# Kernel tuning notes

Measured on AMD Instinct MI355X. Metric: run time of the kernel, lower is better.

The kernel has to match this reference:

```python
import jax, jax.numpy as jnp
import numpy as np

BATCH = 16
N_ROIS = 1000
NUM_CLASSES = 81
DET_MAX = 100
MIN_CONF = 0.7
NMS_THRESH = 0.3
BBOX_STD = jnp.array([0.1, 0.1, 0.2, 0.2], jnp.float32)


def setup_inputs() -> dict:
    key = jax.random.key(0)
    k1, k2, k3, k4, k5 = jax.random.split(key, 5)
    # valid normalized boxes (y1,x1,y2,x2) with y2>y1, x2>x1
    y1 = jax.random.uniform(k1, (BATCH, N_ROIS, 1)) * 0.7
    x1 = jax.random.uniform(k2, (BATCH, N_ROIS, 1)) * 0.7
    hw = jax.random.uniform(k3, (BATCH, N_ROIS, 2)) * 0.28 + 0.02
    rois = jnp.concatenate([y1, x1, y1 + hw[..., :1], x1 + hw[..., 1:]], axis=-1)
    fpn_class = jax.nn.softmax(jax.random.normal(k4, (BATCH, N_ROIS, NUM_CLASSES)) * 2.0, axis=-1)
    fpn_bbox = jax.random.normal(k5, (BATCH, N_ROIS, NUM_CLASSES, 4)) * 0.1
    window = jnp.tile(jnp.array([[0.0, 0.0, 1.0, 1.0]], jnp.float32), (BATCH, 1))
    return {"rois": rois, "fpn_class": fpn_class, "fpn_bbox": fpn_bbox, "window": window}


def apply_box_deltas(boxes, deltas):
    # boxes [N,4] (y1,x1,y2,x2), deltas [N,4] (dy,dx,log dh,log dw)
    h = boxes[:, 2] - boxes[:, 0]
    w = boxes[:, 3] - boxes[:, 1]
    cy = boxes[:, 0] + 0.5 * h
    cx = boxes[:, 1] + 0.5 * w
    cy = cy + deltas[:, 0] * h
    cx = cx + deltas[:, 1] * w
    h = h * jnp.exp(deltas[:, 2])
    w = w * jnp.exp(deltas[:, 3])
    y1 = cy - 0.5 * h
    x1 = cx - 0.5 * w
    return jnp.stack([y1, x1, y1 + h, x1 + w], axis=1)


def clip_boxes(boxes, window):
    wy1, wx1, wy2, wx2 = window[0], window[1], window[2], window[3]
    y1 = jnp.clip(boxes[:, 0], wy1, wy2)
    x1 = jnp.clip(boxes[:, 1], wx1, wx2)
    y2 = jnp.clip(boxes[:, 2], wy1, wy2)
    x2 = jnp.clip(boxes[:, 3], wx1, wx2)
    return jnp.stack([y1, x1, y2, x2], axis=1)


def box_iou(a, b):
    # a [N,4], b [M,4] -> [N,M]
    y1 = jnp.maximum(a[:, None, 0], b[None, :, 0])
    x1 = jnp.maximum(a[:, None, 1], b[None, :, 1])
    y2 = jnp.minimum(a[:, None, 2], b[None, :, 2])
    x2 = jnp.minimum(a[:, None, 3], b[None, :, 3])
    inter = jnp.maximum(y2 - y1, 0.0) * jnp.maximum(x2 - x1, 0.0)
    area_a = (a[:, 2] - a[:, 0]) * (a[:, 3] - a[:, 1])
    area_b = (b[:, 2] - b[:, 0]) * (b[:, 3] - b[:, 1])
    union = area_a[:, None] + area_b[None, :] - inter
    return inter / jnp.maximum(union, 1e-10)


def per_class_nms_mask(boxes, class_ids, scores):
    """boxes [N,4], class_ids [N] int, scores [N] (already -1 where pre-filtered).
    Returns bool [N]: survives greedy per-class NMS (max DET_MAX kept per class)."""
    fg = jnp.arange(1, NUM_CLASSES)                       # [C-1] skip background
    sc = jnp.where(class_ids[None, :] == fg[:, None], scores[None, :], -1.0)  # [C-1,N]
    order = jnp.argsort(-sc, axis=1)                      # [C-1,N] score-desc per class
    iou = box_iou(boxes, boxes)                           # [N,N]
    col = jnp.arange(N_ROIS)
    active0 = sc >= 0.0
    kept0 = jnp.zeros_like(active0)
    cnt0 = jnp.zeros((NUM_CLASSES - 1,), jnp.int32)

    def body(i, carry):
        active, kept, cnt = carry
        cur = order[:, i]                                  # [C-1] current box idx per class
        is_act = jnp.take_along_axis(active, cur[:, None], axis=1)[:, 0]
        is_kept = is_act & (cnt < DET_MAX)
        cnt = cnt + is_kept.astype(jnp.int32)
        kept = kept | ((col[None, :] == cur[:, None]) & is_kept[:, None])
        suppress = is_kept[:, None] & (iou[cur] > NMS_THRESH)  # [C-1,N]
        active = active & ~suppress
        return (active, kept, cnt)

    _, kept, _ = jax.lax.fori_loop(0, N_ROIS, body, (active0, kept0, cnt0))
    return kept.any(axis=0)


def _refine_one(rois, probs, deltas, window):
    n = jnp.arange(N_ROIS)
    class_ids = jnp.argmax(probs, axis=1)                 # [N]
    class_scores = probs[n, class_ids]                    # [N]
    d = deltas[n, class_ids] * BBOX_STD                   # [N,4]
    refined = clip_boxes(apply_box_deltas(rois, d), window)
    keep = (class_ids > 0) & (class_scores >= MIN_CONF)
    sg = jax.lax.stop_gradient
    nms_keep = per_class_nms_mask(
        sg(refined), class_ids, jnp.where(keep, sg(class_scores), -1.0))
    keep = keep & nms_keep
    sf = jnp.where(keep, class_scores, -1.0)
    top_s, top_i = jax.lax.top_k(sf, DET_MAX)             # keep top DET_MAX overall
    valid = top_s >= 0.0
    det = jnp.concatenate(
        [refined[top_i],
         class_ids[top_i][:, None].astype(jnp.float32),
         class_scores[top_i][:, None]], axis=1)           # [DET_MAX,6]
    return jnp.where(valid[:, None], det, 0.0)            # zero-pad invalid rows


def reference(rois, fpn_class, fpn_bbox, window):
    # [B, DET_MAX, 6] = (y1,x1,y2,x2,class_id,score), normalized coords
    return jax.vmap(_refine_one)(rois, fpn_class, fpn_bbox, window)
```

## Files before the change

### kernel.cpp

```cpp
#include <hip/hip_runtime.h>
#include <math.h>

#define BATCH 16
#define N_ROIS 1000
#define NUM_CLASSES 81
#define DET_MAX 100
#define MIN_CONF 0.7f
#define NMS_THRESH 0.3f

#define ROI_TILE 128
#define SUP_WORDS 4

__global__ __launch_bounds__(256) void refine_v4(
    const float* __restrict__ rois, const float* __restrict__ probs,
    const float* __restrict__ deltas, const float* __restrict__ window,
    float* __restrict__ ws_box, float* __restrict__ ws_score, int* __restrict__ ws_cls)
{
    __shared__ float s_probs[ROI_TILE * NUM_CLASSES];

    const int base_roi = blockIdx.x * ROI_TILE;

    const float4* src = (const float4*)(probs + (size_t)base_roi * NUM_CLASSES);
    float4* dst = (float4*)s_probs;
    for (int i = threadIdx.x; i < ROI_TILE * NUM_CLASSES / 4; i += 256)
        dst[i] = src[i];
    __syncthreads();

    if (threadIdx.x < ROI_TILE) {
        const int idx = base_roi + threadIdx.x;
        const int b = idx / N_ROIS;

        const float* p = s_probs + threadIdx.x * NUM_CLASSES;
        float bs0 = p[0], bs1 = p[1], bs2 = p[2], bs3 = p[3];
        int ib0 = 0, ib1 = 1, ib2 = 2, ib3 = 3;
        #pragma unroll
        for (int c = 4; c <= 76; c += 4) {
            float v0 = p[c], v1 = p[c + 1], v2 = p[c + 2], v3 = p[c + 3];
            if (v0 > bs0) { bs0 = v0; ib0 = c; }
            if (v1 > bs1) { bs1 = v1; ib1 = c + 1; }
            if (v2 > bs2) { bs2 = v2; ib2 = c + 2; }
            if (v3 > bs3) { bs3 = v3; ib3 = c + 3; }
        }
        { float v = p[80]; if (v > bs0) { bs0 = v; ib0 = 80; } }
        if (bs1 > bs0 || (bs1 == bs0 && ib1 < ib0)) { bs0 = bs1; ib0 = ib1; }
        if (bs3 > bs2 || (bs3 == bs2 && ib3 < ib2)) { bs2 = bs3; ib2 = ib3; }
        if (bs2 > bs0 || (bs2 == bs0 && ib2 < ib0)) { bs0 = bs2; ib0 = ib2; }
        const float bs = bs0;
        const int best = ib0;

        const bool keep = (best > 0) && (bs >= MIN_CONF);
        ws_score[idx] = keep ? bs : -1.0f;

        if (keep) {
            const float4 dd = ((const float4*)deltas)[(size_t)idx * NUM_CLASSES + best];
            float dy = dd.x * 0.1f, dx = dd.y * 0.1f, dh = dd.z * 0.2f, dw = dd.w * 0.2f;

            const float4 rr = ((const float4*)rois)[idx];
            float y1 = rr.x, x1 = rr.y, y2 = rr.z, x2 = rr.w;
            float h = y2 - y1, w = x2 - x1;
            float cy = y1 + 0.5f * h, cx = x1 + 0.5f * w;
            cy += dy * h;
            cx += dx * w;
            h *= expf(dh);
            w *= expf(dw);
            float ny1 = cy - 0.5f * h;
            float nx1 = cx - 0.5f * w;
            float ny2 = ny1 + h;
            float nx2 = nx1 + w;

            const float* win = window + b * 4;
            float wy1 = win[0], wx1 = win[1], wy2 = win[2], wx2 = win[3];
            ny1 = fminf(fmaxf(ny1, wy1), wy2);
            nx1 = fminf(fmaxf(nx1, wx1), wx2);
            ny2 = fminf(fmaxf(ny2, wy1), wy2);
            nx2 = fminf(fmaxf(nx2, wx1), wx2);

            ((float4*)ws_box)[idx] = make_float4(ny1, nx1, ny2, nx2);
            ws_cls[idx] = best;
        }
    }
}

__global__ __launch_bounds__(256) void nms_v5(
    const float* __restrict__ ws_box, const float* __restrict__ ws_score,
    const int* __restrict__ ws_cls, float* __restrict__ out)
{
    const int b = blockIdx.x;
    const int tid = threadIdx.x;

    __shared__ float s_cbox[N_ROIS][4];
    __shared__ float s_csc[N_ROIS];
    __shared__ short s_cidx[N_ROIS];
    __shared__ unsigned char s_ccls[N_ROIS];
    __shared__ float s_sbox[N_ROIS][4];
    __shared__ float s_ssc[N_ROIS];
    __shared__ unsigned char s_scls[N_ROIS];
    __shared__ unsigned char s_kept[N_ROIS];
    __shared__ short s_bucket[N_ROIS];
    __shared__ short s_pos[N_ROIS];
    __shared__ unsigned long long s_sup[N_ROIS][SUP_WORDS];
    __shared__ int s_cnt[NUM_CLASSES];
    __shared__ int s_off[NUM_CLASSES];
    __shared__ int s_C;

    if (tid == 0) s_C = 0;
    if (tid < NUM_CLASSES) s_cnt[tid] = 0;

    for (int i = tid; i < DET_MAX * 6; i += 256)
        out[(size_t)b * DET_MAX * 6 + i] = 0.0f;
    __syncthreads();

    for (int i = tid; i < N_ROIS; i += 256) {
        float sc = ws_score[b * N_ROIS + i];
        if (sc >= 0.0f) {
            int k = atomicAdd(&s_C, 1);
            s_csc[k] = sc;
            s_cidx[k] = (short)i;
            int c = ws_cls[b * N_ROIS + i];
            s_ccls[k] = (unsigned char)c;
            atomicAdd(&s_cnt[c], 1);
            float4 bb = ((const float4*)ws_box)[b * N_ROIS + i];
            s_cbox[k][0] = bb.x; s_cbox[k][1] = bb.y;
            s_cbox[k][2] = bb.z; s_cbox[k][3] = bb.w;
        }
    }
    __syncthreads();
    const int C = s_C;

    if (tid == 0) {
        int acc = 0;
        for (int c = 0; c < NUM_CLASSES; ++c) { s_off[c] = acc; acc += s_cnt[c]; }
    }
    __syncthreads();

    for (int k = tid; k < C; k += 256) {
        float sk = s_csc[k];
        int ik = s_cidx[k];
        int ck = s_ccls[k];
        int rank = 0, crank = 0;
        for (int j = 0; j < C; ++j) {
            float sj = s_csc[j];
            int before = (sj > sk) | ((sj == sk) & (s_cidx[j] < ik));
            rank += before;
            crank += before & (s_ccls[j] == ck);
        }
        s_ssc[rank] = sk;
        s_scls[rank] = (unsigned char)ck;
        s_sbox[rank][0] = s_cbox[k][0];
        s_sbox[rank][1] = s_cbox[k][1];
        s_sbox[rank][2] = s_cbox[k][2];
        s_sbox[rank][3] = s_cbox[k][3];
        s_kept[rank] = 0;
        s_pos[rank] = (short)crank;
        s_bucket[s_off[ck] + crank] = (short)rank;
    }
    __syncthreads();

    for (int u = tid; u < C; u += 256) {
        const int i = s_bucket[u];
        const int c = s_scls[i];
        const int m = s_cnt[c];
        if (m > 64 * SUP_WORDS) continue;
        const int a = s_pos[i];
        const int off = u - a;
        const float b0 = s_sbox[i][0], b1 = s_sbox[i][1];
        const float b2 = s_sbox[i][2], b3 = s_sbox[i][3];
        const float area_b = (b2 - b0) * (b3 - b1);
        #pragma unroll
        for (int qw = 0; qw < SUP_WORDS; ++qw) {
            unsigned long long w = 0;
            const int qlo = (qw << 6) > (a + 1) ? (qw << 6) : (a + 1);
            const int qhi = m < ((qw << 6) + 64) ? m : ((qw << 6) + 64);
            for (int q = qlo; q < qhi; ++q) {
                const int j = s_bucket[off + q];
                const float a0 = s_sbox[j][0], a1 = s_sbox[j][1];
                const float a2 = s_sbox[j][2], a3 = s_sbox[j][3];
                float yy1 = fmaxf(a0, b0);
                float xx1 = fmaxf(a1, b1);
                float yy2 = fminf(a2, b2);
                float xx2 = fminf(a3, b3);
                float inter = fmaxf(yy2 - yy1, 0.0f) * fmaxf(xx2 - xx1, 0.0f);
                float area_a = (a2 - a0) * (a3 - a1);
                float uni = area_a + area_b - inter;
                w |= (unsigned long long)(inter / fmaxf(uni, 1e-10f) > NMS_THRESH)
                     << (q & 63);
            }
            s_sup[u][qw] = w;
        }
    }
    __syncthreads();

    if (tid >= 1 && tid < NUM_CLASSES) {
        const int off = s_off[tid];
        const int m = s_cnt[tid];
        if (m <= 64 * SUP_WORDS) {
            unsigned long long r0 = 0, r1 = 0, r2 = 0, r3 = 0;
            int cnt = 0;
            for (int a = 0; a < m; ++a) {
                if (cnt >= DET_MAX) break;
                const unsigned long long rb =
                    (a < 64) ? r0 : (a < 128) ? r1 : (a < 192) ? r2 : r3;
                if ((rb >> (a & 63)) & 1ull) continue;
                const int i = s_bucket[off + a];
                s_kept[i] = 1; ++cnt;
                r0 |= s_sup[off + a][0];
                r1 |= s_sup[off + a][1];
                r2 |= s_sup[off + a][2];
                r3 |= s_sup[off + a][3];
            }
        } else {
            int kept_cnt = 0;
            for (int a = 0; a < m; ++a) {
                if (kept_cnt >= DET_MAX) break;
                int i = s_bucket[off + a];
                float b0 = s_sbox[i][0], b1 = s_sbox[i][1];
                float b2 = s_sbox[i][2], b3 = s_sbox[i][3];
                float area_b = (b2 - b0) * (b3 - b1);
                bool sup = false;
                for (int q = 0; q < a; ++q) {
                    int j = s_bucket[off + q];
                    if (!s_kept[j]) continue;
                    float a0 = s_sbox[j][0], a1 = s_sbox[j][1];
                    float a2 = s_sbox[j][2], a3 = s_sbox[j][3];
                    float yy1 = fmaxf(a0, b0);
                    float xx1 = fmaxf(a1, b1);
                    float yy2 = fminf(a2, b2);
                    float xx2 = fminf(a3, b3);
                    float inter = fmaxf(yy2 - yy1, 0.0f) * fmaxf(xx2 - xx1, 0.0f);
                    float area_a = (a2 - a0) * (a3 - a1);
                    float uni = area_a + area_b - inter;
                    if (inter / fmaxf(uni, 1e-10f) > NMS_THRESH) { sup = true; break; }
                }
                if (!sup) { s_kept[i] = 1; ++kept_cnt; }
            }
        }
    }
    __syncthreads();

    for (int i = tid; i < C; i += 256) {
        if (s_kept[i]) {
            int slot = 0;
            for (int j = 0; j < i; ++j) slot += s_kept[j];
            if (slot < DET_MAX) {
                float* o = out + (size_t)b * DET_MAX * 6 + slot * 6;
                o[0] = s_sbox[i][0];
                o[1] = s_sbox[i][1];
                o[2] = s_sbox[i][2];
                o[3] = s_sbox[i][3];
                o[4] = (float)s_scls[i];
                o[5] = s_ssc[i];
            }
        }
    }
}

extern "C" void kernel_launch(void* const* d_in, const int* in_sizes, int n_in,
                              void* d_out, int out_size, void* d_ws, size_t ws_size,
                              hipStream_t stream) {
    const float* rois      = (const float*)d_in[0];
    const float* fpn_class = (const float*)d_in[1];
    const float* fpn_bbox  = (const float*)d_in[2];
    const float* window    = (const float*)d_in[3];
    float* out = (float*)d_out;

    float* ws_box   = (float*)d_ws;
    float* ws_score = ws_box + (size_t)BATCH * N_ROIS * 4;
    int*   ws_cls   = (int*)(ws_score + (size_t)BATCH * N_ROIS);

    refine_v4<<<BATCH * N_ROIS / ROI_TILE, 256, 0, stream>>>(
        rois, fpn_class, fpn_bbox, window, ws_box, ws_score, ws_cls);
    nms_v5<<<BATCH, 256, 0, stream>>>(ws_box, ws_score, ws_cls, out);
}
```

Baseline: 85.72 us.

## Fuse box refinement into per-batch NMS kernel and widen blocks to 512

Merges the argmax/box-refinement kernel into the NMS kernel so each batch block computes candidates directly into shared memory. This removes a second kernel launch and the global workspace write/read of boxes, scores and classes. Block size grows to 512 threads to spread the per-batch work. The tradeoff is that the probability scan now runs on only 16 blocks, with uncoalesced per-thread row reads instead of a grid-wide coalesced tile load.

```diff
diff --git a/kernel.cpp b/kernel.cpp
--- a/kernel.cpp
+++ b/kernel.cpp
@@ -8,82 +8,13 @@
 #define MIN_CONF 0.7f
 #define NMS_THRESH 0.3f
 
-#define ROI_TILE 128
+#define NTHREADS 512
 #define SUP_WORDS 4
 
-__global__ __launch_bounds__(256) void refine_v4(
+__global__ __launch_bounds__(NTHREADS) void detect_fused_v7(
     const float* __restrict__ rois, const float* __restrict__ probs,
     const float* __restrict__ deltas, const float* __restrict__ window,
-    float* __restrict__ ws_box, float* __restrict__ ws_score, int* __restrict__ ws_cls)
-{
-    __shared__ float s_probs[ROI_TILE * NUM_CLASSES];
-
-    const int base_roi = blockIdx.x * ROI_TILE;
-
-    const float4* src = (const float4*)(probs + (size_t)base_roi * NUM_CLASSES);
-    float4* dst = (float4*)s_probs;
-    for (int i = threadIdx.x; i < ROI_TILE * NUM_CLASSES / 4; i += 256)
-        dst[i] = src[i];
-    __syncthreads();
-
-    if (threadIdx.x < ROI_TILE) {
-        const int idx = base_roi + threadIdx.x;
-        const int b = idx / N_ROIS;
-
-        const float* p = s_probs + threadIdx.x * NUM_CLASSES;
-        float bs0 = p[0], bs1 = p[1], bs2 = p[2], bs3 = p[3];
-        int ib0 = 0, ib1 = 1, ib2 = 2, ib3 = 3;
-        #pragma unroll
-        for (int c = 4; c <= 76; c += 4) {
-            float v0 = p[c], v1 = p[c + 1], v2 = p[c + 2], v3 = p[c + 3];
-            if (v0 > bs0) { bs0 = v0; ib0 = c; }
-            if (v1 > bs1) { bs1 = v1; ib1 = c + 1; }
-            if (v2 > bs2) { bs2 = v2; ib2 = c + 2; }
-            if (v3 > bs3) { bs3 = v3; ib3 = c + 3; }
-        }
-        { float v = p[80]; if (v > bs0) { bs0 = v; ib0 = 80; } }
-        if (bs1 > bs0 || (bs1 == bs0 && ib1 < ib0)) { bs0 = bs1; ib0 = ib1; }
-        if (bs3 > bs2 || (bs3 == bs2 && ib3 < ib2)) { bs2 = bs3; ib2 = ib3; }
-        if (bs2 > bs0 || (bs2 == bs0 && ib2 < ib0)) { bs0 = bs2; ib0 = ib2; }
-        const float bs = bs0;
-        const int best = ib0;
-
-        const bool keep = (best > 0) && (bs >= MIN_CONF);
-        ws_score[idx] = keep ? bs : -1.0f;
-
-        if (keep) {
-            const float4 dd = ((const float4*)deltas)[(size_t)idx * NUM_CLASSES + best];
-            float dy = dd.x * 0.1f, dx = dd.y * 0.1f, dh = dd.z * 0.2f, dw = dd.w * 0.2f;
-
-            const float4 rr = ((const float4*)rois)[idx];
-            float y1 = rr.x, x1 = rr.y, y2 = rr.z, x2 = rr.w;
-            float h = y2 - y1, w = x2 - x1;
-            float cy = y1 + 0.5f * h, cx = x1 + 0.5f * w;
-            cy += dy * h;
-            cx += dx * w;
-            h *= expf(dh);
-            w *= expf(dw);
-            float ny1 = cy - 0.5f * h;
-            float nx1 = cx - 0.5f * w;
-            float ny2 = ny1 + h;
-            float nx2 = nx1 + w;
-
-            const float* win = window + b * 4;
-            float wy1 = win[0], wx1 = win[1], wy2 = win[2], wx2 = win[3];
-            ny1 = fminf(fmaxf(ny1, wy1), wy2);
-            nx1 = fminf(fmaxf(nx1, wx1), wx2);
-            ny2 = fminf(fmaxf(ny2, wy1), wy2);
-            nx2 = fminf(fmaxf(nx2, wx1), wx2);
-
-            ((float4*)ws_box)[idx] = make_float4(ny1, nx1, ny2, nx2);
-            ws_cls[idx] = best;
-        }
-    }
-}
-
-__global__ __launch_bounds__(256) void nms_v5(
-    const float* __restrict__ ws_box, const float* __restrict__ ws_score,
-    const int* __restrict__ ws_cls, float* __restrict__ out)
+    float* __restrict__ out)
 {
     const int b = blockIdx.x;
     const int tid = threadIdx.x;
@@ -106,22 +37,61 @@
     if (tid == 0) s_C = 0;
     if (tid < NUM_CLASSES) s_cnt[tid] = 0;
 
-    for (int i = tid; i < DET_MAX * 6; i += 256)
+    for (int i = tid; i < DET_MAX * 6; i += NTHREADS)
         out[(size_t)b * DET_MAX * 6 + i] = 0.0f;
-    __syncthreads();
-
-    for (int i = tid; i < N_ROIS; i += 256) {
-        float sc = ws_score[b * N_ROIS + i];
-        if (sc >= 0.0f) {
-            int k = atomicAdd(&s_C, 1);
-            s_csc[k] = sc;
-            s_cidx[k] = (short)i;
-            int c = ws_cls[b * N_ROIS + i];
-            s_ccls[k] = (unsigned char)c;
-            atomicAdd(&s_cnt[c], 1);
-            float4 bb = ((const float4*)ws_box)[b * N_ROIS + i];
-            s_cbox[k][0] = bb.x; s_cbox[k][1] = bb.y;
-            s_cbox[k][2] = bb.z; s_cbox[k][3] = bb.w;
+
+    const float4 wv = ((const float4*)window)[b];
+    __syncthreads();
+
+    for (int r = tid; r < N_ROIS; r += NTHREADS) {
+        const size_t gidx = (size_t)b * N_ROIS + r;
+        const float* p = probs + gidx * NUM_CLASSES;
+
+        float bs0 = p[0], bs1 = p[1], bs2 = p[2], bs3 = p[3];
+        int ib0 = 0, ib1 = 1, ib2 = 2, ib3 = 3;
+        #pragma unroll
+        for (int c = 4; c <= 76; c += 4) {
+            float v0 = p[c], v1 = p[c + 1], v2 = p[c + 2], v3 = p[c + 3];
+            if (v0 > bs0) { bs0 = v0; ib0 = c; }
+            if (v1 > bs1) { bs1 = v1; ib1 = c + 1; }
+            if (v2 > bs2) { bs2 = v2; ib2 = c + 2; }
+            if (v3 > bs3) { bs3 = v3; ib3 = c + 3; }
+        }
+        { float v = p[80]; if (v > bs0) { bs0 = v; ib0 = 80; } }
+        if (bs1 > bs0 || (bs1 == bs0 && ib1 < ib0)) { bs0 = bs1; ib0 = ib1; }
+        if (bs3 > bs2 || (bs3 == bs2 && ib3 < ib2)) { bs2 = bs3; ib2 = ib3; }
+        if (bs2 > bs0 || (bs2 == bs0 && ib2 < ib0)) { bs0 = bs2; ib0 = ib2; }
+        const float bs = bs0;
+        const int best = ib0;
+
+        if ((best > 0) && (bs >= MIN_CONF)) {
+            const float4 dd = ((const float4*)deltas)[gidx * NUM_CLASSES + best];
+            float dy = dd.x * 0.1f, dx = dd.y * 0.1f, dh = dd.z * 0.2f, dw = dd.w * 0.2f;
+
+            const float4 rr = ((const float4*)rois)[gidx];
+            float y1 = rr.x, x1 = rr.y, y2 = rr.z, x2 = rr.w;
+            float h = y2 - y1, w = x2 - x1;
+            float cy = y1 + 0.5f * h, cx = x1 + 0.5f * w;
+            cy += dy * h;
+            cx += dx * w;
+            h *= expf(dh);
+            w *= expf(dw);
+            float ny1 = cy - 0.5f * h;
+            float nx1 = cx - 0.5f * w;
+            float ny2 = ny1 + h;
+            float nx2 = nx1 + w;
+
+            ny1 = fminf(fmaxf(ny1, wv.x), wv.z);
+            nx1 = fminf(fmaxf(nx1, wv.y), wv.w);
+            ny2 = fminf(fmaxf(ny2, wv.x), wv.z);
+            nx2 = fminf(fmaxf(nx2, wv.y), wv.w);
+
+            const int k = atomicAdd(&s_C, 1);
+            s_csc[k] = bs;
+            s_cidx[k] = (short)r;
+            s_ccls[k] = (unsigned char)best;
+            atomicAdd(&s_cnt[best], 1);
+            ((float4*)s_cbox)[k] = make_float4(ny1, nx1, ny2, nx2);
         }
     }
     __syncthreads();
@@ -133,7 +103,7 @@
     }
     __syncthreads();
 
-    for (int k = tid; k < C; k += 256) {
+    for (int k = tid; k < C; k += NTHREADS) {
         float sk = s_csc[k];
         int ik = s_cidx[k];
         int ck = s_ccls[k];
@@ -146,17 +116,14 @@
         }
         s_ssc[rank] = sk;
         s_scls[rank] = (unsigned char)ck;
-        s_sbox[rank][0] = s_cbox[k][0];
-        s_sbox[rank][1] = s_cbox[k][1];
-        s_sbox[rank][2] = s_cbox[k][2];
-        s_sbox[rank][3] = s_cbox[k][3];
+        ((float4*)s_sbox)[rank] = ((const float4*)s_cbox)[k];
         s_kept[rank] = 0;
         s_pos[rank] = (short)crank;
         s_bucket[s_off[ck] + crank] = (short)rank;
     }
     __syncthreads();
 
-    for (int u = tid; u < C; u += 256) {
+    for (int u = tid; u < C; u += NTHREADS) {
         const int i = s_bucket[u];
         const int c = s_scls[i];
         const int m = s_cnt[c];
@@ -237,7 +204,7 @@
     }
     __syncthreads();
 
-    for (int i = tid; i < C; i += 256) {
+    for (int i = tid; i < C; i += NTHREADS) {
         if (s_kept[i]) {
             int slot = 0;
             for (int j = 0; j < i; ++j) slot += s_kept[j];
@@ -262,12 +229,8 @@
     const float* fpn_bbox  = (const float*)d_in[2];
     const float* window    = (const float*)d_in[3];
     float* out = (float*)d_out;
-
-    float* ws_box   = (float*)d_ws;
-    float* ws_score = ws_box + (size_t)BATCH * N_ROIS * 4;
-    int*   ws_cls   = (int*)(ws_score + (size_t)BATCH * N_ROIS);
-
-    refine_v4<<<BATCH * N_ROIS / ROI_TILE, 256, 0, stream>>>(
-        rois, fpn_class, fpn_bbox, window, ws_box, ws_score, ws_cls);
-    nms_v5<<<BATCH, 256, 0, stream>>>(ws_box, ws_score, ws_cls, out);
+    (void)d_ws; (void)ws_size;
+
+    detect_fused_v7<<<BATCH, NTHREADS, 0, stream>>>(
+        rois, fpn_class, fpn_bbox, window, out);
 }
```

Measured after the change: 87.89 us. +2.5%, slower.
